# Kernel optimization log

Measured on AMD Instinct MI355X. Metric: run time of the kernel, lower is better.

## Reference

```python
import jax, jax.numpy as jnp
import numpy as np

B, N, DIM = 4, 1024, 1024
H, D = 16, 64          # num_heads, head_dim
SW = 256               # sliding_window
ROPE_BASE = 10000.0
LN_EPS = 1e-5


def _layernorm(x, w, b):
    mu = jnp.mean(x, axis=-1, keepdims=True)
    var = jnp.mean((x - mu) ** 2, axis=-1, keepdims=True)
    return (x - mu) * jax.lax.rsqrt(var + LN_EPS) * w + b


def _rotate_half(x):
    x1, x2 = jnp.split(x, 2, axis=-1)
    return jnp.concatenate([-x2, x1], axis=-1)


def setup_inputs() -> dict:
    key = jax.random.key(0)
    ks = jax.random.split(key, 8)
    s = 0.02
    return {
        "x": jax.random.normal(ks[0], (B, N, DIM), dtype=jnp.float32),
        "qkv_w": jax.random.normal(ks[1], (3 * H * D, DIM), dtype=jnp.float32) * s,
        "qn_w": jnp.ones((D,), jnp.float32),
        "qn_b": jnp.zeros((D,), jnp.float32),
        "kn_w": jnp.ones((D,), jnp.float32),
        "kn_b": jnp.zeros((D,), jnp.float32),
        "sinks": jax.random.normal(ks[2], (H,), dtype=jnp.float32),
        "proj_w": jax.random.normal(ks[3], (DIM, H * D), dtype=jnp.float32) * s,
        "proj_b": jnp.zeros((DIM,), jnp.float32),
    }


def reference(x, qkv_w, qn_w, qn_b, kn_w, kn_b, sinks, proj_w, proj_b):
    Bx, Nx, _ = x.shape
    # fused QKV projection -> [3, B, H, N, D]
    qkv = (x @ qkv_w.T).reshape(Bx, Nx, 3, H, D).transpose(2, 0, 3, 1, 4)
    q, k, v = qkv[0], qkv[1], qkv[2]
    # qk-norm (LayerNorm over head_dim)
    q = _layernorm(q, qn_w, qn_b)
    k = _layernorm(k, kn_w, kn_b)
    # 1d RoPE (DeepseekV3-style: emb = cat(freqs, freqs), rotate_half)
    inv_freq = 1.0 / (ROPE_BASE ** (jnp.arange(0, D, 2, dtype=jnp.float32) / D))
    freqs = jnp.arange(Nx, dtype=jnp.float32)[:, None] * inv_freq[None, :]  # [N, D/2]
    emb = jnp.concatenate([freqs, freqs], axis=-1)                           # [N, D]
    cos, sin = jnp.cos(emb), jnp.sin(emb)
    q = q * cos + _rotate_half(q) * sin
    k = k * cos + _rotate_half(k) * sin
    # sliding-window causal mask with attention sinks
    sm_scale = 1.0 / np.sqrt(D)
    scores = jnp.einsum("bhqd,bhkd->bhqk", q, k) * sm_scale  # [B,H,N,N]
    i = jnp.arange(Nx)[:, None]
    j = jnp.arange(Nx)[None, :]
    allowed = (j <= i) & (j > i - SW)
    scores = jnp.where(allowed, scores, -jnp.inf)
    # append sink logit per head, softmax, drop sink column
    sink_col = jnp.broadcast_to(sinks[None, :, None, None], (Bx, H, Nx, 1))
    logits = jnp.concatenate([scores, sink_col], axis=-1)
    probs = jax.nn.softmax(logits, axis=-1)[..., :-1]
    out = jnp.einsum("bhqk,bhkd->bhqd", probs, v)
    out = out.transpose(0, 2, 1, 3).reshape(Bx, Nx, H * D)
    return out @ proj_w.T + proj_b
```

## Files before the change

### kernel.cpp

```cpp
#include <hip/hip_runtime.h>
#include <stdint.h>

typedef unsigned short u16;
typedef __bf16 bf16x8 __attribute__((ext_vector_type(8)));
typedef float f32x4 __attribute__((ext_vector_type(4)));

__device__ __forceinline__ float b2f(u16 u) {
  union { uint32_t i; float f; } x; x.i = ((uint32_t)u) << 16; return x.f;
}
__device__ __forceinline__ u16 f2b(float f) {
  union { float f; uint32_t i; } x; x.f = f;
  uint32_t r = x.i + 0x7fffu + ((x.i >> 16) & 1u);
  return (u16)(r >> 16);
}
__device__ __forceinline__ uint4 pk8(const float4 a, const float4 b) {
  uint4 r;
  r.x = (uint32_t)f2b(a.x) | ((uint32_t)f2b(a.y) << 16);
  r.y = (uint32_t)f2b(a.z) | ((uint32_t)f2b(a.w) << 16);
  r.z = (uint32_t)f2b(b.x) | ((uint32_t)f2b(b.y) << 16);
  r.w = (uint32_t)f2b(b.z) | ((uint32_t)f2b(b.w) << 16);
  return r;
}
__device__ __forceinline__ void gload_lds16(const u16* g, u16* l) {
  __builtin_amdgcn_global_load_lds(
      (const __attribute__((address_space(1))) void*)g,
      (__attribute__((address_space(3))) void*)l, 16, 0, 0);
}

__launch_bounds__(256)
__global__ void prep(const float* __restrict__ x, const float* __restrict__ wq,
                     const float* __restrict__ wp, u16* __restrict__ dst,
                     float* __restrict__ tab) {
  if (blockIdx.x >= 4096) {
    const int tid = (blockIdx.x - 4096) * 256 + threadIdx.x;
    const int pos = tid >> 5, idx = tid & 31;
    const float f = pos * exp2f(idx * -0.41524101186092029f);
    float s, c;
    sincosf(f, &s, &c);
    *(float2*)(tab + tid * 2) = make_float2(c, s);
    return;
  }
  const int i = (blockIdx.x * 256 + threadIdx.x) * 8;
  const float* src; int local, base;
  if (i < 4194304)      { src = x;  local = i;           base = 0; }
  else if (i < 7340032) { src = wq; local = i - 4194304; base = 4194304; }
  else                  { src = wp; local = i - 7340032; base = 7340032; }
  const int row = local >> 10, col = local & 1023;
  const int slot = (((col >> 3) & 3) + (row >> 1)) & 3;
  const float4 a = *(const float4*)(src + local);
  const float4 b = *(const float4*)(src + local + 4);
  *(uint4*)(dst + base + (row << 10) + (col & ~31) + (slot << 3)) = pk8(a, b);
}

__launch_bounds__(256)
__global__ void gemm_qkv(const u16* __restrict__ A, const u16* __restrict__ Bw,
                         u16* __restrict__ Cp, u16* __restrict__ vt, int K) {
  __shared__ __align__(16) u16 As[128 * 32];
  __shared__ __align__(16) u16 Bs[128 * 32];
  const int t = threadIdx.x;
  const int w = t >> 6, l = t & 63, lr = l & 15, lg = l >> 4;
  const int m0 = blockIdx.y * 128, n0 = blockIdx.x * 128;
  const int wm = (w >> 1) * 64, wn = (w & 1) * 64;
  const int srow = w * 32 + (l >> 2);
  const int scol = (l & 3) * 8;
  const u16* ga0 = A  + (m0 + srow) * K + scol;
  const u16* ga1 = ga0 + 16 * K;
  const u16* gb0 = Bw + (n0 + srow) * K + scol;
  const u16* gb1 = gb0 + 16 * K;
  u16* la0 = As + w * 1024;
  u16* la1 = As + w * 1024 + 512;
  u16* lb0 = Bs + w * 1024;
  u16* lb1 = Bs + w * 1024 + 512;

  f32x4 acc[4][4] = {};
  const int nk = K >> 5;
  for (int kt = 0; kt < nk; ++kt) {
    const int ko = kt * 32;
    __syncthreads();
    gload_lds16(ga0 + ko, la0);
    gload_lds16(ga1 + ko, la1);
    gload_lds16(gb0 + ko, lb0);
    gload_lds16(gb1 + ko, lb1);
    __syncthreads();
    bf16x8 af[4], bfr[4];
#pragma unroll
    for (int i = 0; i < 4; ++i) {
      const int ra = wm + i * 16 + lr;
      af[i] = *(const bf16x8*)(As + ra * 32 + (((lg + (ra >> 1)) & 3) << 3));
    }
#pragma unroll
    for (int j = 0; j < 4; ++j) {
      const int rb = wn + j * 16 + lr;
      bfr[j] = *(const bf16x8*)(Bs + rb * 32 + (((lg + (rb >> 1)) & 3) << 3));
    }
#pragma unroll
    for (int i = 0; i < 4; ++i)
#pragma unroll
      for (int j = 0; j < 4; ++j)
        acc[i][j] = __builtin_amdgcn_mfma_f32_16x16x32_bf16(af[i], bfr[j], acc[i][j], 0, 0, 0);
  }
  const int whichB = blockIdx.x >> 3;
  const int hh = ((n0 + wn) >> 6) & 15;
  if (whichB == 2) {
#pragma unroll
    for (int i = 0; i < 4; ++i)
#pragma unroll
      for (int j = 0; j < 4; ++j)
#pragma unroll
        for (int r = 0; r < 4; ++r) {
          const int gm = m0 + wm + i * 16 + lg * 4 + r;
          const int bh = (gm >> 10) * 16 + hh;
          const int pos = gm & 1023, nb = pos >> 6, jl = pos & 63;
          const int d = j * 16 + lr;
          vt[bh * 65536 + nb * 4096 + d * 64 + (((jl >> 3) ^ (d & 7)) << 3) + (jl & 7)] =
              f2b(acc[i][j][r]);
        }
    return;
  }
  u16* Cb = Cp + whichB * 4194304;
#pragma unroll
  for (int i = 0; i < 4; ++i)
#pragma unroll
    for (int j = 0; j < 4; ++j)
#pragma unroll
      for (int r = 0; r < 4; ++r) {
        const int gm = m0 + wm + i * 16 + lg * 4 + r;
        Cb[(((gm >> 10) * 16 + hh) << 16) + ((gm & 1023) << 6) + j * 16 + lr] =
            f2b(acc[i][j][r]);
      }
}

__launch_bounds__(256)
__global__ void ln_rope(u16* __restrict__ qk, const float* __restrict__ qn_w,
                        const float* __restrict__ qn_b, const float* __restrict__ kn_w,
                        const float* __restrict__ kn_b, const float* __restrict__ tab) {
  const int t = threadIdx.x, l = t & 63;
  const int wv = blockIdx.x * 4 + (t >> 6);
  const int row = wv * 8 + (l >> 3);
  const int c = l & 7;
  const int which = row >> 16;
  const int pos = row & 1023;
  const float* wgt = which ? kn_w : qn_w;
  const float* bia = which ? kn_b : qn_b;
  const u16* src = qk + row * 64 + c * 8;
  const ushort4 ra = *(const ushort4*)(src);
  const ushort4 rb = *(const ushort4*)(src + 4);
  float v[8] = {b2f(ra.x), b2f(ra.y), b2f(ra.z), b2f(ra.w),
                b2f(rb.x), b2f(rb.y), b2f(rb.z), b2f(rb.w)};
  float s = 0.f;
#pragma unroll
  for (int i = 0; i < 8; ++i) s += v[i];
#pragma unroll
  for (int off = 1; off < 8; off <<= 1) s += __shfl_xor(s, off);
  const float mu = s * 0.015625f;
  float e[8], qs = 0.f;
#pragma unroll
  for (int i = 0; i < 8; ++i) { e[i] = v[i] - mu; qs += e[i] * e[i]; }
#pragma unroll
  for (int off = 1; off < 8; off <<= 1) qs += __shfl_xor(qs, off);
  const float rstd = rsqrtf(qs * 0.015625f + 1e-5f);
  const int d0 = c * 8;
  float wb[8], bb[8];
  *(float4*)(wb) = *(const float4*)(wgt + d0);
  *(float4*)(wb + 4) = *(const float4*)(wgt + d0 + 4);
  *(float4*)(bb) = *(const float4*)(bia + d0);
  *(float4*)(bb + 4) = *(const float4*)(bia + d0 + 4);
  float n[8], r[8];
#pragma unroll
  for (int i = 0; i < 8; ++i) n[i] = e[i] * rstd * wb[i] + bb[i];
#pragma unroll
  for (int i = 0; i < 8; ++i) r[i] = __shfl_xor(n[i], 4);
  const bool lo = (c < 4);
#pragma unroll
  for (int i = 0; i < 8; ++i) r[i] = lo ? -r[i] : r[i];
  float cs[16];
  const int ti = (pos * 32 + (c & 3) * 8) * 2;
  *(float4*)(cs)      = *(const float4*)(tab + ti);
  *(float4*)(cs + 4)  = *(const float4*)(tab + ti + 4);
  *(float4*)(cs + 8)  = *(const float4*)(tab + ti + 8);
  *(float4*)(cs + 12) = *(const float4*)(tab + ti + 12);
  ushort4 oa, ob;
  float o[8];
#pragma unroll
  for (int i = 0; i < 8; ++i) o[i] = n[i] * cs[2 * i] + r[i] * cs[2 * i + 1];
  oa.x = f2b(o[0]); oa.y = f2b(o[1]); oa.z = f2b(o[2]); oa.w = f2b(o[3]);
  ob.x = f2b(o[4]); ob.y = f2b(o[5]); ob.z = f2b(o[6]); ob.w = f2b(o[7]);
  const int dstc = which ? (c ^ (pos & 7)) : c;
  u16* dst = qk + row * 64 + dstc * 8;
  *(ushort4*)(dst) = oa;
  *(ushort4*)(dst + 4) = ob;
}

__launch_bounds__(256)
__global__ void gemm_proj(const u16* __restrict__ A, const u16* __restrict__ Bw,
                          float* __restrict__ out, const float* __restrict__ bias,
                          int K) {
  __shared__ __align__(16) u16 As[128 * 32];
  __shared__ __align__(16) u16 Bs[64 * 32];
  const int t = threadIdx.x;
  const int w = t >> 6, l = t & 63, lr = l & 15, lg = l >> 4;
  const int m0 = blockIdx.y * 128, n0 = blockIdx.x * 64;
  const int wm = (w >> 1) * 64, wn = (w & 1) * 32;
  const int srowA = w * 32 + (l >> 2);
  const int srowB = w * 16 + (l >> 2);
  const int scol = (l & 3) * 8;
  const u16* ga0 = A  + (m0 + srowA) * K + scol;
  const u16* ga1 = ga0 + 16 * K;
  const u16* gb  = Bw + (n0 + srowB) * K + scol;
  u16* la0 = As + w * 1024;
  u16* la1 = As + w * 1024 + 512;
  u16* lb  = Bs + w * 512;

  f32x4 acc[4][2] = {};
  const int nk = K >> 5;
  for (int kt = 0; kt < nk; ++kt) {
    const int ko = kt * 32;
    __syncthreads();
    gload_lds16(ga0 + ko, la0);
    gload_lds16(ga1 + ko, la1);
    gload_lds16(gb + ko, lb);
    __syncthreads();
    bf16x8 af[4], bfr[2];
#pragma unroll
    for (int i = 0; i < 4; ++i) {
      const int ra = wm + i * 16 + lr;
      af[i] = *(const bf16x8*)(As + ra * 32 + (((lg + (ra >> 1)) & 3) << 3));
    }
#pragma unroll
    for (int j = 0; j < 2; ++j) {
      const int rb = wn + j * 16 + lr;
      bfr[j] = *(const bf16x8*)(Bs + rb * 32 + (((lg + (rb >> 1)) & 3) << 3));
    }
#pragma unroll
    for (int i = 0; i < 4; ++i)
#pragma unroll
      for (int j = 0; j < 2; ++j)
        acc[i][j] = __builtin_amdgcn_mfma_f32_16x16x32_bf16(af[i], bfr[j], acc[i][j], 0, 0, 0);
  }
#pragma unroll
  for (int i = 0; i < 4; ++i)
#pragma unroll
    for (int j = 0; j < 2; ++j)
#pragma unroll
      for (int r = 0; r < 4; ++r) {
        const int gm = m0 + wm + i * 16 + lg * 4 + r;
        const int gn = n0 + wn + j * 16 + lr;
        out[(gm << 10) + gn] = acc[i][j][r] + bias[gn];
      }
}

__launch_bounds__(256, 2)
__global__ void attn_kernel(const u16* __restrict__ q, const u16* __restrict__ k,
                            const u16* __restrict__ vt, const float* __restrict__ sinks,
                            u16* __restrict__ ao) {
  __shared__ __align__(16) u16 Ks[20480];
  __shared__ __align__(16) u16 Vs[20480];
  const int t = threadIdx.x, w = t >> 6, l = t & 63, lr = l & 15, lg = l >> 4;
  const int bid = blockIdx.x;
  const int qb = bid & 15, h = (bid >> 4) & 15, b = bid >> 8;
  const int i0 = qb * 64 + w * 16;
  const int bh = b * 16 + h;
  const u16* qp = q + bh * 65536;
  const u16* kp = k + bh * 65536;
  const u16* vp = vt + bh * 65536;
  const int j0 = qb * 64 - 256;

#pragma unroll
  for (int i = 0; i < 10; ++i) {
    const int c = w * 10 + i;
    int off = j0 * 64 + c * 512 + l * 8;
    off = off < 0 ? 0 : off;
    gload_lds16(kp + off, Ks + c * 512);
  }
#pragma unroll
  for (int i = 0; i < 10; ++i) {
    const int c = w * 10 + i;
    const int n = c >> 3, p = c & 7;
    int nb = qb - 4 + n;
    nb = nb < 0 ? 0 : nb;
    gload_lds16(vp + nb * 4096 + p * 512 + l * 8, Vs + c * 512);
  }
  const bf16x8 qf0 = *(const bf16x8*)(qp + (i0 + lr) * 64 + lg * 8);
  const bf16x8 qf1 = *(const bf16x8*)(qp + (i0 + lr) * 64 + 32 + lg * 8);
  __syncthreads();

  const int key = lr & 7;
  f32x4 sacc[17];
#pragma unroll
  for (int jt = 0; jt < 17; ++jt) {
    const int r = w * 16 + jt * 16 + lr;
    const bf16x8 kf0 = *(const bf16x8*)(Ks + r * 64 + ((lg ^ key)) * 8);
    const bf16x8 kf1 = *(const bf16x8*)(Ks + r * 64 + (((lg + 4) ^ key)) * 8);
    f32x4 a = {0.f, 0.f, 0.f, 0.f};
    a = __builtin_amdgcn_mfma_f32_16x16x32_bf16(qf0, kf0, a, 0, 0, 0);
    a = __builtin_amdgcn_mfma_f32_16x16x32_bf16(qf1, kf1, a, 0, 0, 0);
    sacc[jt] = a;
  }
  const float sink = sinks[h];
  const int ja = i0 - 256;
  float mx[4] = {-1e30f, -1e30f, -1e30f, -1e30f};
#pragma unroll
  for (int jt = 0; jt < 17; ++jt)
#pragma unroll
    for (int r = 0; r < 4; ++r) {
      const int qi = i0 + lg * 4 + r;
      const int jg = ja + jt * 16 + lr;
      const bool ok = (jg >= 0) && (jg <= qi) && (jg > qi - 256);
      const float sv = ok ? sacc[jt][r] * 0.125f : -1e30f;
      sacc[jt][r] = sv;
      mx[r] = fmaxf(mx[r], sv);
    }
#pragma unroll
  for (int off = 1; off < 16; off <<= 1)
#pragma unroll
    for (int r = 0; r < 4; ++r) mx[r] = fmaxf(mx[r], __shfl_xor(mx[r], off));
#pragma unroll
  for (int r = 0; r < 4; ++r) mx[r] = fmaxf(mx[r], sink);
  float sum[4] = {0.f, 0.f, 0.f, 0.f};
#pragma unroll
  for (int jt = 0; jt < 17; ++jt)
#pragma unroll
    for (int r = 0; r < 4; ++r) {
      const float e = __expf(sacc[jt][r] - mx[r]);
      sacc[jt][r] = e;
      sum[r] += e;
    }
#pragma unroll
  for (int off = 1; off < 16; off <<= 1)
#pragma unroll
    for (int r = 0; r < 4; ++r) sum[r] += __shfl_xor(sum[r], off);
  float inv[4];
#pragma unroll
  for (int r = 0; r < 4; ++r) inv[r] = 1.0f / (sum[r] + __expf(sink - mx[r]));

  __syncthreads();
  u16* pb = Ks + w * 4736;
  {
    ushort4 z; z.x = 0; z.y = 0; z.z = 0; z.w = 0;
    *(ushort4*)(pb + (l >> 2) * 296 + 272 + (l & 3) * 4) = z;
  }
#pragma unroll
  for (int jt = 0; jt < 17; ++jt)
#pragma unroll
    for (int r = 0; r < 4; ++r)
      pb[(lg * 4 + r) * 296 + jt * 16 + lr] = f2b(sacc[jt][r] * inv[r]);

  f32x4 oacc[4] = {};
#pragma unroll
  for (int ks = 0; ks < 9; ++ks) {
    const bf16x8 pf = *(const bf16x8*)(pb + lr * 296 + ks * 32 + lg * 8);
#pragma unroll
    for (int dt = 0; dt < 4; ++dt) {
      int r = w * 16 + ks * 32 + lg * 8;
      r = r < 320 ? r : 0;
      const int n = r >> 6, jl = r & 63;
      const int slot = (jl >> 3) ^ (lr & 7);
      const bf16x8 vf = *(const bf16x8*)(Vs + n * 4096 + (dt * 16 + lr) * 64 + slot * 8);
      oacc[dt] = __builtin_amdgcn_mfma_f32_16x16x32_bf16(pf, vf, oacc[dt], 0, 0, 0);
    }
  }
#pragma unroll
  for (int dt = 0; dt < 4; ++dt)
#pragma unroll
    for (int r = 0; r < 4; ++r) {
      const int m = (b << 10) + i0 + lg * 4 + r;
      const int d = dt * 16 + lr;
      const int cg = (((d >> 3) & 3) + (m >> 1)) & 3;
      ao[(m << 10) + (h << 6) + (d & ~31) + (cg << 3) + (d & 7)] = f2b(oacc[dt][r]);
    }
}

extern "C" void kernel_launch(void* const* d_in, const int* in_sizes, int n_in,
                              void* d_out, int out_size, void* d_ws, size_t ws_size,
                              hipStream_t stream) {
  const float* x      = (const float*)d_in[0];
  const float* qkv_w  = (const float*)d_in[1];
  const float* qn_w   = (const float*)d_in[2];
  const float* qn_b   = (const float*)d_in[3];
  const float* kn_w   = (const float*)d_in[4];
  const float* kn_b   = (const float*)d_in[5];
  const float* sinks  = (const float*)d_in[6];
  const float* proj_w = (const float*)d_in[7];
  const float* proj_b = (const float*)d_in[8];
  float* out = (float*)d_out;
  u16* ws     = (u16*)d_ws;
  u16* qkv    = ws;
  u16* vtw    = ws + 8388608;
  u16* xb     = ws + 12582912;
  u16* wprojb = ws + 19922944;
  float* tab  = (float*)(ws + 20971520);
  u16* ao     = ws + 21233664;

  prep<<<4224, 256, 0, stream>>>(x, qkv_w, proj_w, xb, tab);
  gemm_qkv<<<dim3(24, 32), 256, 0, stream>>>(xb, xb + 4194304, qkv, vtw, 1024);
  ln_rope<<<4096, 256, 0, stream>>>(qkv, qn_w, qn_b, kn_w, kn_b, tab);
  attn_kernel<<<1024, 256, 0, stream>>>(qkv, qkv + 4194304, vtw, sinks, ao);
  gemm_proj<<<dim3(16, 32), 256, 0, stream>>>(ao, wprojb, out, proj_b, 1024);
}
```

Baseline: 183.2 us.

## Double GEMM K-tile to 64 with XOR swizzled LDS layout

Raises the K step of the QKV and output-projection GEMMs from 32 to 64. This halves the number of sync-separated load/compute iterations and doubles the MFMA work per barrier. The pre-swizzled global layout written by prep and by the attention output changes from a 4-slot rotate to an 8-slot XOR swizzle, so LDS reads from 64-wide rows stay bank-conflict free. LDS use per block doubles, which may lower occupancy.

```diff
diff --git a/kernel.cpp b/kernel.cpp
--- a/kernel.cpp
+++ b/kernel.cpp
@@ -46,58 +46,60 @@
   else if (i < 7340032) { src = wq; local = i - 4194304; base = 4194304; }
   else                  { src = wp; local = i - 7340032; base = 7340032; }
   const int row = local >> 10, col = local & 1023;
-  const int slot = (((col >> 3) & 3) + (row >> 1)) & 3;
+  const int slot = ((col >> 3) & 7) ^ (row & 7);
   const float4 a = *(const float4*)(src + local);
   const float4 b = *(const float4*)(src + local + 4);
-  *(uint4*)(dst + base + (row << 10) + (col & ~31) + (slot << 3)) = pk8(a, b);
+  *(uint4*)(dst + base + (row << 10) + (col & ~63) + (slot << 3)) = pk8(a, b);
 }
 
 __launch_bounds__(256)
 __global__ void gemm_qkv(const u16* __restrict__ A, const u16* __restrict__ Bw,
                          u16* __restrict__ Cp, u16* __restrict__ vt, int K) {
-  __shared__ __align__(16) u16 As[128 * 32];
-  __shared__ __align__(16) u16 Bs[128 * 32];
+  __shared__ __align__(16) u16 As[128 * 64];
+  __shared__ __align__(16) u16 Bs[128 * 64];
   const int t = threadIdx.x;
   const int w = t >> 6, l = t & 63, lr = l & 15, lg = l >> 4;
   const int m0 = blockIdx.y * 128, n0 = blockIdx.x * 128;
   const int wm = (w >> 1) * 64, wn = (w & 1) * 64;
-  const int srow = w * 32 + (l >> 2);
-  const int scol = (l & 3) * 8;
-  const u16* ga0 = A  + (m0 + srow) * K + scol;
-  const u16* ga1 = ga0 + 16 * K;
-  const u16* gb0 = Bw + (n0 + srow) * K + scol;
-  const u16* gb1 = gb0 + 16 * K;
-  u16* la0 = As + w * 1024;
-  u16* la1 = As + w * 1024 + 512;
-  u16* lb0 = Bs + w * 1024;
-  u16* lb1 = Bs + w * 1024 + 512;
+  const int srow = w * 32 + (l >> 3);
+  const int scol = (l & 7) * 8;
+  const u16* gA = A  + (m0 + srow) * K + scol;
+  const u16* gB = Bw + (n0 + srow) * K + scol;
 
   f32x4 acc[4][4] = {};
-  const int nk = K >> 5;
+  const int nk = K >> 6;
   for (int kt = 0; kt < nk; ++kt) {
-    const int ko = kt * 32;
+    const int ko = kt * 64;
     __syncthreads();
-    gload_lds16(ga0 + ko, la0);
-    gload_lds16(ga1 + ko, la1);
-    gload_lds16(gb0 + ko, lb0);
-    gload_lds16(gb1 + ko, lb1);
+#pragma unroll
+    for (int i = 0; i < 4; ++i)
+      gload_lds16(gA + i * 8 * K + ko, As + (w * 32 + i * 8) * 64);
+#pragma unroll
+    for (int i = 0; i < 4; ++i)
+      gload_lds16(gB + i * 8 * K + ko, Bs + (w * 32 + i * 8) * 64);
     __syncthreads();
-    bf16x8 af[4], bfr[4];
+    bf16x8 af0[4], af1[4], bf0[4], bf1[4];
 #pragma unroll
     for (int i = 0; i < 4; ++i) {
       const int ra = wm + i * 16 + lr;
-      af[i] = *(const bf16x8*)(As + ra * 32 + (((lg + (ra >> 1)) & 3) << 3));
+      const int sa = (lg ^ (ra & 7)) * 8;
+      af0[i] = *(const bf16x8*)(As + ra * 64 + sa);
+      af1[i] = *(const bf16x8*)(As + ra * 64 + (sa ^ 32));
     }
 #pragma unroll
     for (int j = 0; j < 4; ++j) {
       const int rb = wn + j * 16 + lr;
-      bfr[j] = *(const bf16x8*)(Bs + rb * 32 + (((lg + (rb >> 1)) & 3) << 3));
-    }
-#pragma unroll
-    for (int i = 0; i < 4; ++i)
-#pragma unroll
-      for (int j = 0; j < 4; ++j)
-        acc[i][j] = __builtin_amdgcn_mfma_f32_16x16x32_bf16(af[i], bfr[j], acc[i][j], 0, 0, 0);
+      const int sb = (lg ^ (rb & 7)) * 8;
+      bf0[j] = *(const bf16x8*)(Bs + rb * 64 + sb);
+      bf1[j] = *(const bf16x8*)(Bs + rb * 64 + (sb ^ 32));
+    }
+#pragma unroll
+    for (int i = 0; i < 4; ++i)
+#pragma unroll
+      for (int j = 0; j < 4; ++j) {
+        acc[i][j] = __builtin_amdgcn_mfma_f32_16x16x32_bf16(af0[i], bf0[j], acc[i][j], 0, 0, 0);
+        acc[i][j] = __builtin_amdgcn_mfma_f32_16x16x32_bf16(af1[i], bf1[j], acc[i][j], 0, 0, 0);
+      }
   }
   const int whichB = blockIdx.x >> 3;
   const int hh = ((n0 + wn) >> 6) & 15;
@@ -195,47 +197,52 @@
 __global__ void gemm_proj(const u16* __restrict__ A, const u16* __restrict__ Bw,
                           float* __restrict__ out, const float* __restrict__ bias,
                           int K) {
-  __shared__ __align__(16) u16 As[128 * 32];
-  __shared__ __align__(16) u16 Bs[64 * 32];
+  __shared__ __align__(16) u16 As[128 * 64];
+  __shared__ __align__(16) u16 Bs[64 * 64];
   const int t = threadIdx.x;
   const int w = t >> 6, l = t & 63, lr = l & 15, lg = l >> 4;
   const int m0 = blockIdx.y * 128, n0 = blockIdx.x * 64;
   const int wm = (w >> 1) * 64, wn = (w & 1) * 32;
-  const int srowA = w * 32 + (l >> 2);
-  const int srowB = w * 16 + (l >> 2);
-  const int scol = (l & 3) * 8;
-  const u16* ga0 = A  + (m0 + srowA) * K + scol;
-  const u16* ga1 = ga0 + 16 * K;
-  const u16* gb  = Bw + (n0 + srowB) * K + scol;
-  u16* la0 = As + w * 1024;
-  u16* la1 = As + w * 1024 + 512;
-  u16* lb  = Bs + w * 512;
+  const int srowA = w * 32 + (l >> 3);
+  const int srowB = w * 16 + (l >> 3);
+  const int scol = (l & 7) * 8;
+  const u16* gA = A  + (m0 + srowA) * K + scol;
+  const u16* gB = Bw + (n0 + srowB) * K + scol;
 
   f32x4 acc[4][2] = {};
-  const int nk = K >> 5;
+  const int nk = K >> 6;
   for (int kt = 0; kt < nk; ++kt) {
-    const int ko = kt * 32;
+    const int ko = kt * 64;
     __syncthreads();
-    gload_lds16(ga0 + ko, la0);
-    gload_lds16(ga1 + ko, la1);
-    gload_lds16(gb + ko, lb);
+#pragma unroll
+    for (int i = 0; i < 4; ++i)
+      gload_lds16(gA + i * 8 * K + ko, As + (w * 32 + i * 8) * 64);
+#pragma unroll
+    for (int i = 0; i < 2; ++i)
+      gload_lds16(gB + i * 8 * K + ko, Bs + (w * 16 + i * 8) * 64);
     __syncthreads();
-    bf16x8 af[4], bfr[2];
+    bf16x8 af0[4], af1[4], bf0[2], bf1[2];
 #pragma unroll
     for (int i = 0; i < 4; ++i) {
       const int ra = wm + i * 16 + lr;
-      af[i] = *(const bf16x8*)(As + ra * 32 + (((lg + (ra >> 1)) & 3) << 3));
+      const int sa = (lg ^ (ra & 7)) * 8;
+      af0[i] = *(const bf16x8*)(As + ra * 64 + sa);
+      af1[i] = *(const bf16x8*)(As + ra * 64 + (sa ^ 32));
     }
 #pragma unroll
     for (int j = 0; j < 2; ++j) {
       const int rb = wn + j * 16 + lr;
-      bfr[j] = *(const bf16x8*)(Bs + rb * 32 + (((lg + (rb >> 1)) & 3) << 3));
-    }
-#pragma unroll
-    for (int i = 0; i < 4; ++i)
-#pragma unroll
-      for (int j = 0; j < 2; ++j)
-        acc[i][j] = __builtin_amdgcn_mfma_f32_16x16x32_bf16(af[i], bfr[j], acc[i][j], 0, 0, 0);
+      const int sb = (lg ^ (rb & 7)) * 8;
+      bf0[j] = *(const bf16x8*)(Bs + rb * 64 + sb);
+      bf1[j] = *(const bf16x8*)(Bs + rb * 64 + (sb ^ 32));
+    }
+#pragma unroll
+    for (int i = 0; i < 4; ++i)
+#pragma unroll
+      for (int j = 0; j < 2; ++j) {
+        acc[i][j] = __builtin_amdgcn_mfma_f32_16x16x32_bf16(af0[i], bf0[j], acc[i][j], 0, 0, 0);
+        acc[i][j] = __builtin_amdgcn_mfma_f32_16x16x32_bf16(af1[i], bf1[j], acc[i][j], 0, 0, 0);
+      }
   }
 #pragma unroll
   for (int i = 0; i < 4; ++i)
@@ -364,9 +371,8 @@
 #pragma unroll
     for (int r = 0; r < 4; ++r) {
       const int m = (b << 10) + i0 + lg * 4 + r;
-      const int d = dt * 16 + lr;
-      const int cg = (((d >> 3) & 3) + (m >> 1)) & 3;
-      ao[(m << 10) + (h << 6) + (d & ~31) + (cg << 3) + (d & 7)] = f2b(oacc[dt][r]);
+      const int cg = (dt * 2 + (lr >> 3)) ^ (m & 7);
+      ao[(m << 10) + (h << 6) + (cg << 3) + (lr & 7)] = f2b(oacc[dt][r]);
     }
 }
 
```

Result: faster. 175.4 us (median of 2 runs) (-4.3%).
